# Kernel tuning notes

Measured on AMD Instinct MI355X. Metric: run time of the kernel, lower is better.

The kernel has to match this reference:

```python
import jax, jax.numpy as jnp
import numpy as np

B, S, H = 2, 1024, 4544
NH, HD = 71, 64          # 71 query heads, head_dim 64, 1 shared kv head (multi-query)
THETA = 10000.0
NEG_INF = -1e9


def setup_inputs() -> dict:
    key = jax.random.key(0)
    k1, k2, k3 = jax.random.split(key, 3)
    hidden_states = jax.random.normal(k1, (B, S, H), dtype=jnp.float32)
    W_qkv = jax.random.normal(k2, (H, H + 2 * HD), dtype=jnp.float32) * 0.02
    W_dense = jax.random.normal(k3, (H, H), dtype=jnp.float32) * 0.02
    causal = jnp.tril(jnp.ones((S, S), dtype=bool))
    attention_mask = jnp.where(causal, 0.0, NEG_INF).astype(jnp.float32)[None, None]  # [1,1,S,S]
    position_ids = jnp.arange(S, dtype=jnp.int32)[None]  # [1,S]
    return {"hidden_states": hidden_states, "W_qkv": W_qkv, "W_dense": W_dense,
            "attention_mask": attention_mask, "position_ids": position_ids}


def _rope_cos_sin(position_ids):
    # HF FalconRotaryEmbedding: inv_freq over even dims, emb = cat(freqs, freqs)
    inv_freq = 1.0 / (THETA ** (jnp.arange(0, HD, 2, dtype=jnp.float32) / HD))
    freqs = position_ids.astype(jnp.float32)[..., None] * inv_freq  # [1,S,HD/2]
    emb = jnp.concatenate([freqs, freqs], axis=-1)                  # [1,S,HD]
    return jnp.cos(emb)[:, None], jnp.sin(emb)[:, None]             # [1,1,S,HD]


def _rotate_half(x):
    return jnp.concatenate([-x[..., HD // 2:], x[..., :HD // 2]], axis=-1)


def reference(hidden_states, W_qkv, W_dense, attention_mask, position_ids):
    # fused QKV projection (bias=False for Falcon-7B)
    fused = hidden_states @ W_qkv                       # [B,S,(NH+2)*HD]
    fused = fused.reshape(B, S, NH + 2, HD)
    q = jnp.transpose(fused[:, :, :NH], (0, 2, 1, 3))          # [B,NH,S,HD]
    k = jnp.transpose(fused[:, :, NH:NH + 1], (0, 2, 1, 3))    # [B,1,S,HD]
    v = jnp.transpose(fused[:, :, NH + 1:], (0, 2, 1, 3))      # [B,1,S,HD]

    cos, sin = _rope_cos_sin(position_ids)
    q = q * cos + _rotate_half(q) * sin
    k = k * cos + _rotate_half(k) * sin

    # scores: shared kv head broadcasts across the 71 query heads
    scores = jnp.matmul(q, jnp.swapaxes(k, -1, -2)) * (1.0 / np.sqrt(HD))  # [B,NH,S,S]
    probs = jax.nn.softmax(scores + attention_mask, axis=-1)
    attn = jnp.matmul(probs, v)                                            # [B,NH,S,HD]

    attn = jnp.transpose(attn, (0, 2, 1, 3)).reshape(B, S, NH * HD)
    return attn @ W_dense
```

## Files before the change

kernel.cpp:

```cpp
#include <hip/hip_runtime.h>

typedef unsigned short u16;
using f32x4  = __attribute__((ext_vector_type(4))) float;
using f32x16 = __attribute__((ext_vector_type(16))) float;
using s16x8  = __attribute__((ext_vector_type(8))) short;

static __device__ __forceinline__ u16 f2b(float f) {
  unsigned int u = __builtin_bit_cast(unsigned int, f);
  u = (u + 0x7fffu + ((u >> 16) & 1u)) >> 16;
  return (u16)u;
}
static __device__ __forceinline__ unsigned int cvtpk(float lo, float hi) {
  unsigned int r;
  asm("v_cvt_pk_bf16_f32 %0, %1, %2" : "=v"(r) : "v"(lo), "v"(hi));
  return r;
}
static __device__ __forceinline__ void gload16(const void* g, void* l) {
  __builtin_amdgcn_global_load_lds(
      (const __attribute__((address_space(1))) void*)g,
      (__attribute__((address_space(3))) void*)l, 16, 0, 0);
}

template<int NT>
static __device__ __forceinline__ void transpose_tile(
    const float* __restrict__ W, u16* __restrict__ Wt, int K, int N,
    int n0, int k0, int t, u16 (*tile)[72])
{
  #pragma unroll
  for (int i = 0; i < 1024 / NT; ++i) {
    int idx = i * NT + t;
    int r = idx >> 4;
    int c = (idx & 15) << 2;
    float4 v = make_float4(0.f, 0.f, 0.f, 0.f);
    if (n0 + c < N) v = *(const float4*)(W + (size_t)(k0 + r) * N + n0 + c);
    tile[r][c + 0] = f2b(v.x);
    tile[r][c + 1] = f2b(v.y);
    tile[r][c + 2] = f2b(v.z);
    tile[r][c + 3] = f2b(v.w);
  }
  __syncthreads();
  #pragma unroll
  for (int i = 0; i < 512 / NT; ++i) {
    int idx = i * NT + t;
    int rn = idx >> 3;
    int c8 = (idx & 7) << 3;
    __align__(16) u16 tmp[8];
    #pragma unroll
    for (int j = 0; j < 8; ++j) tmp[j] = tile[c8 + j][rn];
    *(uint4*)(Wt + (size_t)(n0 + rn) * K + k0 + c8) = *(const uint4*)tmp;
  }
}

__global__ __launch_bounds__(256) void prep_kernel(
    const float* __restrict__ hidden, u16* __restrict__ A1,
    const float* __restrict__ Wqkv, u16* __restrict__ Wt)
{
  __shared__ u16 tile[64][72];
  const int bid = blockIdx.x, t = threadIdx.x;
  if (bid < 4544) {
    int i = bid * 256 + t;
    float4 a = *(const float4*)(hidden + (size_t)i * 8);
    float4 b = *(const float4*)(hidden + (size_t)i * 8 + 4);
    __align__(16) u16 tmp[8] = {f2b(a.x), f2b(a.y), f2b(a.z), f2b(a.w),
                                f2b(b.x), f2b(b.y), f2b(b.z), f2b(b.w)};
    *(uint4*)(A1 + (size_t)i * 8) = *(const uint4*)tmp;
  } else {
    int tb = bid - 4544;
    int n0 = (tb % 74) * 64, k0 = (tb / 74) * 64;
    transpose_tile<256>(Wqkv, Wt, 4544, 4672, n0, k0, t, tile);
  }
}

template<int MODE>
__global__ __launch_bounds__(256) void gemm_bt(
    const u16* __restrict__ A, const u16* __restrict__ B,
    float* __restrict__ Cptr,
    u16* __restrict__ qo, u16* __restrict__ ko, u16* __restrict__ vo,
    const int* __restrict__ pos,
    int M, int N, int K, int NBX)
{
  __shared__ __align__(16) u16 aLds[2][128 * 32];
  __shared__ __align__(16) u16 bLds[2][128 * 32];

  const int t = threadIdx.x, lane = t & 63, w = t >> 6;
  const int lr = lane & 15, lg = lane >> 4;
  const int wr = w >> 1, wc = w & 1;

  const int bid = blockIdx.x;
  const int qq  = gridDim.x >> 3;
  const int swz = (bid & 7) * qq + (bid >> 3);
  const int m0 = (swz / NBX) * 128, n0 = (swz % NBX) * 128;

  const int srow = lane >> 2;
  const int ssl  = ((lane & 3) ^ ((lane >> 3) & 3)) << 3;

  f32x4 acc[4][4] = {};
  const int nk = K >> 5;

#define STAGE(buf, tt) do {                                                   \
    size_t kq_ = (size_t)(tt) << 5;                                           \
    _Pragma("unroll")                                                         \
    for (int i_ = 0; i_ < 2; ++i_) {                                          \
      int row_ = i_ * 64 + w * 16 + srow;                                     \
      gload16(A + (size_t)(m0 + row_) * K + kq_ + ssl,                        \
              (char*)&aLds[buf][0] + i_ * 4096 + w * 1024);                   \
      gload16(B + (size_t)(n0 + row_) * K + kq_ + ssl,                        \
              (char*)&bLds[buf][0] + i_ * 4096 + w * 1024);                   \
    }                                                                         \
  } while (0)

  STAGE(0, 0);

  const int sl = (lg ^ ((lr >> 1) & 3)) << 3;
  for (int kt = 0; kt < nk; ++kt) {
    const int cur = kt & 1;
    if (kt + 1 < nk) {
      STAGE(cur ^ 1, kt + 1);
      asm volatile("s_waitcnt vmcnt(4)" ::: "memory");
    } else {
      asm volatile("s_waitcnt vmcnt(0)" ::: "memory");
    }
    __builtin_amdgcn_s_barrier();
    __builtin_amdgcn_sched_barrier(0);
    const u16* ab = &aLds[cur][0];
    const u16* bb = &bLds[cur][0];
    s16x8 af[4], bf[4];
    #pragma unroll
    for (int m = 0; m < 4; ++m)
      af[m] = *(const s16x8*)(ab + (wr * 64 + m * 16 + lr) * 32 + sl);
    #pragma unroll
    for (int n = 0; n < 4; ++n)
      bf[n] = *(const s16x8*)(bb + (wc * 64 + n * 16 + lr) * 32 + sl);
    #pragma unroll
    for (int m = 0; m < 4; ++m)
      #pragma unroll
      for (int n = 0; n < 4; ++n)
        acc[m][n] = __builtin_amdgcn_mfma_f32_16x16x32_bf16(af[m], bf[n], acc[m][n], 0, 0, 0);
    __builtin_amdgcn_s_barrier();
  }
#undef STAGE

  if constexpr (MODE == 0) {
    #pragma unroll
    for (int m = 0; m < 4; ++m) {
      int row = m0 + wr * 64 + m * 16 + lg * 4;
      #pragma unroll
      for (int n = 0; n < 4; ++n) {
        int col = n0 + wc * 64 + n * 16 + lr;
        if (col < N) {
          #pragma unroll
          for (int r = 0; r < 4; ++r)
            Cptr[(size_t)(row + r) * N + col] = acc[m][n][r];
        }
      }
    }
  } else {
    const int h = (n0 + wc * 64) >> 6;
    if (h > 72) return;
    const float inv0 = exp2f(-0.41524101186092029f * (float)lr);
    const float inv1 = exp2f(-0.41524101186092029f * (float)(16 + lr));
    #pragma unroll
    for (int m = 0; m < 4; ++m) {
      #pragma unroll
      for (int r = 0; r < 4; ++r) {
        int row = m0 + wr * 64 + m * 16 + lg * 4 + r;
        int b = row >> 10, s = row & 1023;
        if (h == 72) {
          #pragma unroll
          for (int n = 0; n < 4; ++n) {
            int d = n * 16 + lr;
            vo[((size_t)b * 64 + d) * 1024 + s] = f2b(acc[m][n][r]);
          }
        } else {
          float p = (float)pos[s];
          float sn0, cs0, sn1, cs1;
          __sincosf(p * inv0, &sn0, &cs0);
          __sincosf(p * inv1, &sn1, &cs1);
          #pragma unroll
          for (int n = 0; n < 4; ++n) {
            float cs  = (n & 1) ? cs1 : cs0;
            float sn  = (n & 1) ? sn1 : sn0;
            float sgn = (n < 2) ? -1.f : 1.f;
            float val = acc[m][n][r] * cs + sgn * acc[m][n ^ 2][r] * sn;
            int d = n * 16 + lr;
            if (h < 71)
              qo[((size_t)(b * 71 + h) * 1024 + s) * 64 + d] = f2b(val);
            else
              ko[((size_t)b * 1024 + s) * 64 + d] = f2b(val);
          }
        }
      }
    }
  }
}

__global__ __launch_bounds__(128) void attn_plus(
    const u16* __restrict__ q, const u16* __restrict__ kx,
    const u16* __restrict__ vT, u16* __restrict__ attnO,
    const float* __restrict__ Wd, u16* __restrict__ Wt)
{
  __shared__ u16 tile[64][72];
  const int bid = blockIdx.x;
  if (bid >= 2272) {
    int tb = bid - 2272;
    int n0 = (tb % 72) * 64, k0 = (tb / 72) * 64;
    transpose_tile<128>(Wd, Wt, 4544, 4544, n0, k0, threadIdx.x, tile);
    return;
  }
  const int t = threadIdx.x, lane = t & 63, w = t >> 6;
  const int lq  = lane & 31;
  const int hi  = lane >> 5;
  const int hi4 = hi << 2;
  const int pair = bid & 15, h = (bid >> 4) % 71, b = bid / 1136;
  const int qt = w ? (31 - pair) : pair;
  const int q0 = qt * 32;

  const u16* qbase = q + ((size_t)(b * 71 + h) * 1024 + q0 + lq) * 64 + hi * 8;
  s16x8 qf[4];
  #pragma unroll
  for (int kt = 0; kt < 4; ++kt) qf[kt] = *(const s16x8*)(qbase + kt * 16);

  f32x16 o0 = {}, o1 = {};
  float m = -1e30f, l = 0.f;

  const u16* kbase  = kx + ((size_t)b * 1024 + lq) * 64 + hi * 8;
  const u16* vbase0 = vT + ((size_t)b * 64 + lq) * 1024 + hi * 8;
  const u16* vbase1 = vbase0 + 32 * 1024;

  for (int it = 0; it <= qt; ++it) {
    const int kv0 = it * 32;
    s16x8 kf[4];
    #pragma unroll
    for (int kt = 0; kt < 4; ++kt)
      kf[kt] = *(const s16x8*)(kbase + (size_t)kv0 * 64 + kt * 16);
    s16x8 v00 = *(const s16x8*)(vbase0 + kv0);
    s16x8 v01 = *(const s16x8*)(vbase0 + kv0 + 16);
    s16x8 v10 = *(const s16x8*)(vbase1 + kv0);
    s16x8 v11 = *(const s16x8*)(vbase1 + kv0 + 16);

    f32x16 sa = {}, sb = {};
    sa = __builtin_amdgcn_mfma_f32_32x32x16_bf16(kf[0], qf[0], sa, 0, 0, 0);
    sb = __builtin_amdgcn_mfma_f32_32x32x16_bf16(kf[1], qf[1], sb, 0, 0, 0);
    sa = __builtin_amdgcn_mfma_f32_32x32x16_bf16(kf[2], qf[2], sa, 0, 0, 0);
    sb = __builtin_amdgcn_mfma_f32_32x32x16_bf16(kf[3], qf[3], sb, 0, 0, 0);

    float s[16];
    float pmax = -1e30f;
    if (it == qt) {
      #pragma unroll
      for (int r = 0; r < 16; ++r) {
        int R = (r & 3) + ((r >> 2) << 3) + hi4;
        s[r] = (R > lq) ? -1e30f : (sa[r] + sb[r]) * 0.125f;
        pmax = fmaxf(pmax, s[r]);
      }
    } else {
      #pragma unroll
      for (int r = 0; r < 16; ++r) {
        s[r] = (sa[r] + sb[r]) * 0.125f;
        pmax = fmaxf(pmax, s[r]);
      }
    }
    pmax = fmaxf(pmax, __shfl_xor(pmax, 32));

    if (!__all(pmax <= m + 8.f)) {
      float mn = fmaxf(m, pmax);
      float corr = __expf(m - mn);
      m = mn;
      l *= corr;
      #pragma unroll
      for (int r = 0; r < 16; ++r) {
        float c2 = __shfl(corr, (r & 3) + ((r >> 2) << 3) + hi4);
        o0[r] *= c2; o1[r] *= c2;
      }
    }

    float p[16], sum = 0.f;
    #pragma unroll
    for (int r = 0; r < 16; ++r) { p[r] = __expf(s[r] - m); sum += p[r]; }
    sum += __shfl_xor(sum, 32);
    l += sum;

    unsigned int a0 = cvtpk(p[0], p[1]),   a1 = cvtpk(p[2], p[3]);
    unsigned int b0 = cvtpk(p[4], p[5]),   b1 = cvtpk(p[6], p[7]);
    asm("v_permlane32_swap_b32 %0, %1" : "+v"(a0), "+v"(b0));
    asm("v_permlane32_swap_b32 %0, %1" : "+v"(a1), "+v"(b1));
    unsigned int c0 = cvtpk(p[8], p[9]),   c1 = cvtpk(p[10], p[11]);
    unsigned int d0 = cvtpk(p[12], p[13]), d1 = cvtpk(p[14], p[15]);
    asm("v_permlane32_swap_b32 %0, %1" : "+v"(c0), "+v"(d0));
    asm("v_permlane32_swap_b32 %0, %1" : "+v"(c1), "+v"(d1));
    union { unsigned int wd[4]; s16x8 v; } palo, pahi;
    palo.wd[0] = a0; palo.wd[1] = a1; palo.wd[2] = b0; palo.wd[3] = b1;
    pahi.wd[0] = c0; pahi.wd[1] = c1; pahi.wd[2] = d0; pahi.wd[3] = d1;

    o0 = __builtin_amdgcn_mfma_f32_32x32x16_bf16(palo.v, v00, o0, 0, 0, 0);
    o0 = __builtin_amdgcn_mfma_f32_32x32x16_bf16(pahi.v, v01, o0, 0, 0, 0);
    o1 = __builtin_amdgcn_mfma_f32_32x32x16_bf16(palo.v, v10, o1, 0, 0, 0);
    o1 = __builtin_amdgcn_mfma_f32_32x32x16_bf16(pahi.v, v11, o1, 0, 0, 0);
  }

  float linv = 1.f / l;
  #pragma unroll
  for (int r = 0; r < 16; ++r) {
    int R = (r & 3) + ((r >> 2) << 3) + hi4;
    float c2 = __shfl(linv, R);
    size_t base = ((size_t)(b * 1024 + q0 + R) * 71 + h) * 64;
    attnO[base + lq]      = f2b(o0[r] * c2);
    attnO[base + 32 + lq] = f2b(o1[r] * c2);
  }
}

extern "C" void kernel_launch(void* const* d_in, const int* in_sizes, int n_in,
                              void* d_out, int out_size, void* d_ws, size_t ws_size,
                              hipStream_t stream) {
  const float* hidden = (const float*)d_in[0];
  const float* Wqkv   = (const float*)d_in[1];
  const float* Wdense = (const float*)d_in[2];
  const int*   pos    = (const int*)d_in[4];
  float* out = (float*)d_out;

  char* wsp = (char*)d_ws;
  u16* Wt    = (u16*)(wsp);
  u16* A1    = (u16*)(wsp + 43040768);
  u16* qws   = (u16*)(wsp + 43040768 + 18612224);
  u16* kws   = (u16*)(wsp + 43040768 + 18612224 + 18612224);
  u16* vws   = (u16*)(wsp + 43040768 + 18612224 + 18612224 + 262144);
  u16* attnw = A1;

  prep_kernel<<<4544 + 5254, 256, 0, stream>>>(hidden, A1, Wqkv, Wt);
  gemm_bt<2><<<592, 256, 0, stream>>>(A1, Wt, nullptr, qws, kws, vws, pos,
                                      2048, 4672, 4544, 37);
  attn_plus<<<2272 + 5112, 128, 0, stream>>>(qws, kws, vws, attnw, Wdense, Wt);
  gemm_bt<0><<<576, 256, 0, stream>>>(attnw, Wt, out, nullptr, nullptr, nullptr,
                                      nullptr, 2048, 4544, 4544, 36);
}
```

Baseline: 384.3 us.

## Split K across two wave groups per GEMM block with LDS reduction

Both bf16 GEMMs now launch 512-thread blocks. Two groups of four waves each compute the same 128x128 output tile over separate halves of K, each with its own double-buffered LDS staging. The upper group's partial accumulators pass through LDS in two halves and are added by the lower group, which then runs the original epilogue. The aim is to double the waves per CU for better latency hiding and MFMA utilisation on a small grid. The cost is twice the LDS per block, an extra reduction with barriers, and lower occupancy per block slot.

```diff
diff --git a/kernel.cpp b/kernel.cpp
--- a/kernel.cpp
+++ b/kernel.cpp
@@ -72,19 +72,20 @@
 }
 
 template<int MODE>
-__global__ __launch_bounds__(256) void gemm_bt(
+__global__ __launch_bounds__(512) void gemm_bt(
     const u16* __restrict__ A, const u16* __restrict__ B,
     float* __restrict__ Cptr,
     u16* __restrict__ qo, u16* __restrict__ ko, u16* __restrict__ vo,
     const int* __restrict__ pos,
     int M, int N, int K, int NBX)
 {
-  __shared__ __align__(16) u16 aLds[2][128 * 32];
-  __shared__ __align__(16) u16 bLds[2][128 * 32];
+  __shared__ __align__(16) u16 aLds[2][2][128 * 32];
+  __shared__ __align__(16) u16 bLds[2][2][128 * 32];
 
   const int t = threadIdx.x, lane = t & 63, w = t >> 6;
+  const int wg = w & 3, ks = w >> 2;
   const int lr = lane & 15, lg = lane >> 4;
-  const int wr = w >> 1, wc = w & 1;
+  const int wr = wg >> 1, wc = wg & 1;
 
   const int bid = blockIdx.x;
   const int qq  = gridDim.x >> 3;
@@ -94,18 +95,22 @@
   const int srow = lane >> 2;
   const int ssl  = ((lane & 3) ^ ((lane >> 3) & 3)) << 3;
 
+  const int KH = K >> 1;
+  const int nk = KH >> 5;
+  const u16* Abase = A + (size_t)ks * KH;
+  const u16* Bbase = B + (size_t)ks * KH;
+
   f32x4 acc[4][4] = {};
-  const int nk = K >> 5;
 
 #define STAGE(buf, tt) do {                                                   \
     size_t kq_ = (size_t)(tt) << 5;                                           \
     _Pragma("unroll")                                                         \
     for (int i_ = 0; i_ < 2; ++i_) {                                          \
-      int row_ = i_ * 64 + w * 16 + srow;                                     \
-      gload16(A + (size_t)(m0 + row_) * K + kq_ + ssl,                        \
-              (char*)&aLds[buf][0] + i_ * 4096 + w * 1024);                   \
-      gload16(B + (size_t)(n0 + row_) * K + kq_ + ssl,                        \
-              (char*)&bLds[buf][0] + i_ * 4096 + w * 1024);                   \
+      int row_ = i_ * 64 + wg * 16 + srow;                                    \
+      gload16(Abase + (size_t)(m0 + row_) * K + kq_ + ssl,                    \
+              (char*)&aLds[ks][buf][0] + i_ * 4096 + wg * 1024);              \
+      gload16(Bbase + (size_t)(n0 + row_) * K + kq_ + ssl,                    \
+              (char*)&bLds[ks][buf][0] + i_ * 4096 + wg * 1024);              \
     }                                                                         \
   } while (0)
 
@@ -122,8 +127,8 @@
     }
     __builtin_amdgcn_s_barrier();
     __builtin_amdgcn_sched_barrier(0);
-    const u16* ab = &aLds[cur][0];
-    const u16* bb = &bLds[cur][0];
+    const u16* ab = &aLds[ks][cur][0];
+    const u16* bb = &bLds[ks][cur][0];
     s16x8 af[4], bf[4];
     #pragma unroll
     for (int m = 0; m < 4; ++m)
@@ -139,6 +144,28 @@
     __builtin_amdgcn_s_barrier();
   }
 #undef STAGE
+
+  f32x4* cb = (f32x4*)&aLds[0][0][0];
+  #pragma unroll
+  for (int half = 0; half < 2; ++half) {
+    if (ks == 1) {
+      #pragma unroll
+      for (int mm = 0; mm < 2; ++mm)
+        #pragma unroll
+        for (int n = 0; n < 4; ++n)
+          cb[(wg * 8 + mm * 4 + n) * 64 + lane] = acc[half * 2 + mm][n];
+    }
+    __syncthreads();
+    if (ks == 0) {
+      #pragma unroll
+      for (int mm = 0; mm < 2; ++mm)
+        #pragma unroll
+        for (int n = 0; n < 4; ++n)
+          acc[half * 2 + mm][n] += cb[(wg * 8 + mm * 4 + n) * 64 + lane];
+    }
+    __syncthreads();
+  }
+  if (ks == 1) return;
 
   if constexpr (MODE == 0) {
     #pragma unroll
@@ -327,9 +354,9 @@
   u16* attnw = A1;
 
   prep_kernel<<<4544 + 5254, 256, 0, stream>>>(hidden, A1, Wqkv, Wt);
-  gemm_bt<2><<<592, 256, 0, stream>>>(A1, Wt, nullptr, qws, kws, vws, pos,
+  gemm_bt<2><<<592, 512, 0, stream>>>(A1, Wt, nullptr, qws, kws, vws, pos,
                                       2048, 4672, 4544, 37);
   attn_plus<<<2272 + 5112, 128, 0, stream>>>(qws, kws, vws, attnw, Wdense, Wt);
-  gemm_bt<0><<<576, 256, 0, stream>>>(attnw, Wt, out, nullptr, nullptr, nullptr,
+  gemm_bt<0><<<576, 512, 0, stream>>>(attnw, Wt, out, nullptr, nullptr, nullptr,
                                       nullptr, 2048, 4544, 4544, 36);
 }
```

New measurement: 465.0 us. 1.21x slower.

## Split-K both projection GEMMs in two with separate combine kernels

Applied to the files above, without the earlier changes.

Runs the QKV and dense GEMMs as two half-K partial products, doubling the block count to fill more CUs, then sums the partials in separate kernels. The QKV path moves the RoPE/scatter epilogue into a combine kernel, and the dense path adds the second partial into the output. This trades extra fp32 partial-buffer traffic and two extra launches for better occupancy. It is gated on the workspace being large enough.

```diff
diff --git a/kernel.cpp b/kernel.cpp
--- a/kernel.cpp
+++ b/kernel.cpp
@@ -71,13 +71,13 @@
   }
 }
 
-template<int MODE>
+template<int MODE, int SPLIT>
 __global__ __launch_bounds__(256) void gemm_bt(
     const u16* __restrict__ A, const u16* __restrict__ B,
-    float* __restrict__ Cptr,
+    float* __restrict__ C0, float* __restrict__ C1,
     u16* __restrict__ qo, u16* __restrict__ ko, u16* __restrict__ vo,
     const int* __restrict__ pos,
-    int M, int N, int K, int NBX)
+    int M, int N, int K, int KLEN, int NBX, int CW)
 {
   __shared__ __align__(16) u16 aLds[2][128 * 32];
   __shared__ __align__(16) u16 bLds[2][128 * 32];
@@ -86,25 +86,30 @@
   const int lr = lane & 15, lg = lane >> 4;
   const int wr = w >> 1, wc = w & 1;
 
-  const int bid = blockIdx.x;
-  const int qq  = gridDim.x >> 3;
+  int bid = blockIdx.x, ks = 0;
+  int half = SPLIT ? (gridDim.x >> 1) : gridDim.x;
+  if (SPLIT && bid >= half) { ks = 1; bid -= half; }
+  const int qq  = half >> 3;
   const int swz = (bid & 7) * qq + (bid >> 3);
   const int m0 = (swz / NBX) * 128, n0 = (swz % NBX) * 128;
 
+  const u16* Ab = A + (size_t)ks * KLEN;
+  const u16* Bb = B + (size_t)ks * KLEN;
+
   const int srow = lane >> 2;
   const int ssl  = ((lane & 3) ^ ((lane >> 3) & 3)) << 3;
 
   f32x4 acc[4][4] = {};
-  const int nk = K >> 5;
+  const int nk = KLEN >> 5;
 
 #define STAGE(buf, tt) do {                                                   \
     size_t kq_ = (size_t)(tt) << 5;                                           \
     _Pragma("unroll")                                                         \
     for (int i_ = 0; i_ < 2; ++i_) {                                          \
       int row_ = i_ * 64 + w * 16 + srow;                                     \
-      gload16(A + (size_t)(m0 + row_) * K + kq_ + ssl,                        \
+      gload16(Ab + (size_t)(m0 + row_) * K + kq_ + ssl,                       \
               (char*)&aLds[buf][0] + i_ * 4096 + w * 1024);                   \
-      gload16(B + (size_t)(n0 + row_) * K + kq_ + ssl,                        \
+      gload16(Bb + (size_t)(n0 + row_) * K + kq_ + ssl,                       \
               (char*)&bLds[buf][0] + i_ * 4096 + w * 1024);                   \
     }                                                                         \
   } while (0)
@@ -140,7 +145,8 @@
   }
 #undef STAGE
 
-  if constexpr (MODE == 0) {
+  if constexpr (SPLIT == 1) {
+    float* Cp = ks ? C1 : C0;
     #pragma unroll
     for (int m = 0; m < 4; ++m) {
       int row = m0 + wr * 64 + m * 16 + lg * 4;
@@ -150,7 +156,21 @@
         if (col < N) {
           #pragma unroll
           for (int r = 0; r < 4; ++r)
-            Cptr[(size_t)(row + r) * N + col] = acc[m][n][r];
+            Cp[(size_t)(row + r) * CW + col] = acc[m][n][r];
+        }
+      }
+    }
+  } else if constexpr (MODE == 0) {
+    #pragma unroll
+    for (int m = 0; m < 4; ++m) {
+      int row = m0 + wr * 64 + m * 16 + lg * 4;
+      #pragma unroll
+      for (int n = 0; n < 4; ++n) {
+        int col = n0 + wc * 64 + n * 16 + lr;
+        if (col < N) {
+          #pragma unroll
+          for (int r = 0; r < 4; ++r)
+            C0[(size_t)(row + r) * N + col] = acc[m][n][r];
         }
       }
     }
@@ -194,6 +214,46 @@
   }
 }
 
+__global__ __launch_bounds__(128) void combine_rope(
+    const float* __restrict__ P0, const float* __restrict__ P1,
+    const int* __restrict__ pos,
+    u16* __restrict__ qo, u16* __restrict__ ko, u16* __restrict__ vo)
+{
+  const int col = blockIdx.x * 128 + threadIdx.x;
+  const int row = blockIdx.y;
+  const int h = col >> 6, d = col & 63;
+  if (h >= 73) return;
+  const int b = row >> 10, s = row & 1023;
+  const size_t idx = (size_t)row * 4736 + col;
+  const float v0 = P0[idx] + P1[idx];
+  if (h == 72) {
+    vo[((size_t)b * 64 + d) * 1024 + s] = f2b(v0);
+    return;
+  }
+  const size_t idxp = (size_t)row * 4736 + (col ^ 32);
+  const float vp = P0[idxp] + P1[idxp];
+  const float p = (float)pos[s];
+  const float inv = exp2f(-0.41524101186092029f * (float)(d & 31));
+  float sn, cs;
+  __sincosf(p * inv, &sn, &cs);
+  const float sgn = (d < 32) ? -1.f : 1.f;
+  const float val = v0 * cs + sgn * vp * sn;
+  if (h < 71)
+    qo[((size_t)(b * 71 + h) * 1024 + s) * 64 + d] = f2b(val);
+  else
+    ko[((size_t)b * 1024 + s) * 64 + d] = f2b(val);
+}
+
+__global__ __launch_bounds__(256) void combine_add(
+    float* __restrict__ out, const float* __restrict__ P)
+{
+  size_t i = (size_t)blockIdx.x * 256 + threadIdx.x;
+  float4 a = ((const float4*)out)[i];
+  float4 b = ((const float4*)P)[i];
+  a.x += b.x; a.y += b.y; a.z += b.z; a.w += b.w;
+  ((float4*)out)[i] = a;
+}
+
 __global__ __launch_bounds__(128) void attn_plus(
     const u16* __restrict__ q, const u16* __restrict__ kx,
     const u16* __restrict__ vT, u16* __restrict__ attnO,
@@ -324,12 +384,31 @@
   u16* qws   = (u16*)(wsp + 43040768 + 18612224);
   u16* kws   = (u16*)(wsp + 43040768 + 18612224 + 18612224);
   u16* vws   = (u16*)(wsp + 43040768 + 18612224 + 18612224 + 262144);
+  float* P0  = (float*)(wsp + 80789504);
+  float* P1  = (float*)(wsp + 80789504 + 38797312);
   u16* attnw = A1;
 
+  const bool split = ws_size >= 158384128ull;
+
   prep_kernel<<<4544 + 5254, 256, 0, stream>>>(hidden, A1, Wqkv, Wt);
-  gemm_bt<2><<<592, 256, 0, stream>>>(A1, Wt, nullptr, qws, kws, vws, pos,
-                                      2048, 4672, 4544, 37);
+
+  if (split) {
+    gemm_bt<0, 1><<<1184, 256, 0, stream>>>(A1, Wt, P0, P1,
+        nullptr, nullptr, nullptr, nullptr, 2048, 4736, 4544, 2272, 37, 4736);
+    combine_rope<<<dim3(37, 2048), 128, 0, stream>>>(P0, P1, pos, qws, kws, vws);
+  } else {
+    gemm_bt<2, 0><<<592, 256, 0, stream>>>(A1, Wt, nullptr, nullptr,
+        qws, kws, vws, pos, 2048, 4672, 4544, 4544, 37, 0);
+  }
+
   attn_plus<<<2272 + 5112, 128, 0, stream>>>(qws, kws, vws, attnw, Wdense, Wt);
-  gemm_bt<0><<<576, 256, 0, stream>>>(attnw, Wt, out, nullptr, nullptr, nullptr,
-                                      nullptr, 2048, 4544, 4544, 36);
-}
+
+  if (split) {
+    gemm_bt<0, 1><<<1152, 256, 0, stream>>>(attnw, Wt, out, P0,
+        nullptr, nullptr, nullptr, nullptr, 2048, 4544, 4544, 2272, 36, 4544);
+    combine_add<<<9088, 256, 0, stream>>>(out, P0);
+  } else {
+    gemm_bt<0, 0><<<576, 256, 0, stream>>>(attnw, Wt, out, nullptr,
+        nullptr, nullptr, nullptr, nullptr, 2048, 4544, 4544, 4544, 36, 0);
+  }
+}
```

Result: slower. 461.4 us (+20.1%).
